# Performance work log

Hardware: AMD Instinct MI355X
Metric: run time of the kernel (lower is better)

Reference implementation:

```python
import jax, jax.numpy as jnp
import numpy as np

BANDWIDTH = 0.1
NUM_ITERS = 5


def setup_inputs() -> dict:
    key = jax.random.key(0)
    # image batch in [0,1], BCHW
    x = jax.random.uniform(key, (2, 3, 96, 96), dtype=jnp.float32)
    return {"x": x}


def reference(x):
    # Mean-shift filtering: each pixel feature y is iteratively moved to the
    # Gaussian-kernel weighted mean of ALL original pixel features:
    #   y_{t+1} = sum_j exp(-||y_t - x_j||^2 / (2 bw^2)) x_j / sum_j exp(...)
    B, C, H, W = x.shape
    N = H * W
    pts = x.reshape(B, C, N).transpose(0, 2, 1)  # [B, N, C] original points
    inv2bw2 = jnp.float32(1.0 / (2.0 * BANDWIDTH * BANDWIDTH))
    x_sq = jnp.sum(pts * pts, axis=-1)  # [B, N]

    def step(y, _):
        # squared pairwise distances via ||y||^2 + ||x||^2 - 2 y.x  -> [B, N, N]
        y_sq = jnp.sum(y * y, axis=-1)  # [B, N]
        d2 = y_sq[:, :, None] + x_sq[:, None, :] - 2.0 * jnp.einsum(
            'bnc,bmc->bnm', y, pts)
        w = jnp.exp(-jnp.maximum(d2, 0.0) * inv2bw2)  # Gaussian kernel weights
        num = jnp.einsum('bnm,bmc->bnc', w, pts)  # weighted sum of points
        den = jnp.sum(w, axis=-1, keepdims=True)  # normalizer (>= 1, self-weight)
        return num / den, None

    y, _ = jax.lax.scan(step, pts, None, length=NUM_ITERS)
    return y.transpose(0, 2, 1).reshape(B, C, H, W)
```

## Files before the change

kernel.cpp:

```cpp
#include <hip/hip_runtime.h>
#include <math.h>


typedef float v2f __attribute__((ext_vector_type(2)));

#define NPTS   9216
#define NB     2
#define TOT    (NB * NPTS)
#define MSPLIT 24
#define SLICE  (NPTS / MSPLIT)
#define WSLICE (SLICE / 4)
#define NPB    256
#define NTILES (NPTS / NPB)
#define LOG2E  1.44269504088896340736f
#define BIASF  217.0f
#define T23F   8388608.0f
#define A2F    -2574068.3f
#define B2F    -666404.1f

__device__ __forceinline__ v2f splat2(float v) { return (v2f){v, v}; }


__global__ __launch_bounds__(256, 4) void ms_iter(const float* __restrict__ x,
                                                  const float4* __restrict__ accIn,
                                                  float4* __restrict__ accOut,
                                                  float s, int first) {
    __shared__ float4 smem[1024];
    float* const xs = (float*)smem;
    float* const ys = xs + SLICE;
    float* const zs = ys + SLICE;
    float* const ws = zs + SLICE;
    float4* const ypar = smem + SLICE;
    float4* const red  = smem;

    const int tid  = threadIdx.x;
    const int lane = tid & 63;
    const int wv   = tid >> 6;
    const int k    = blockIdx.x % MSPLIT;
    const int tile = blockIdx.x / MSPLIT;
    const int b    = tile / NTILES;
    const int nt   = tile - b * NTILES;
    const int nbase = nt * NPB;
    const float* xb = x + b * 3 * NPTS;
    const int mbeg = k * SLICE;

    for (int i = tid; i < SLICE; i += 256) {
        int g = mbeg + i;
        float px = xb[g] * s;
        float py = xb[NPTS + g] * s;
        float pz = xb[2 * NPTS + g] * s;
        xs[i] = 2.f * px;
        ys[i] = 2.f * py;
        zs[i] = 2.f * pz;
        ws[i] = -fmaf(px, px, fmaf(py, py, pz * pz));
    }
    {
        float y0, y1, y2;
        if (first) {
            int n = nbase + tid;
            y0 = xb[n] * s; y1 = xb[NPTS + n] * s; y2 = xb[2 * NPTS + n] * s;
        } else {
            float4 a = accIn[b * NPTS + nbase + tid];
            float inv = 1.0f / a.w;
            y0 = a.x * inv; y1 = a.y * inv; y2 = a.z * inv;
        }
        ypar[tid] = make_float4(y0, y1, y2,
                                BIASF - fmaf(y0, y0, fmaf(y1, y1, y2 * y2)));
    }
    __syncthreads();

    v2f Yx[4], Yy[4], Yz[4], Yw[4], Ax[4], Ay[4], Az[4], Aw[4];
#pragma unroll
    for (int j = 0; j < 4; ++j) {
        float4 yp = ypar[lane + 64 * j];
        Yx[j] = splat2(yp.x); Yy[j] = splat2(yp.y);
        Yz[j] = splat2(yp.z); Yw[j] = splat2(yp.w);
        Ax[j] = splat2(0.f); Ay[j] = splat2(0.f);
        Az[j] = splat2(0.f); Aw[j] = splat2(0.f);
    }

    const float* xsw = xs + wv * WSLICE;
    const float* ysw = ys + wv * WSLICE;
    const float* zsw = zs + wv * WSLICE;
    const float* wsw = ws + wv * WSLICE;

    const v2f T23 = splat2(T23F);
    const v2f A2  = splat2(A2F);
    const v2f B2  = splat2(B2F);

    for (int i = 0; i < WSLICE; i += 4) {
        float4 PX = *(const float4*)(xsw + i);
        float4 PY = *(const float4*)(ysw + i);
        float4 PZ = *(const float4*)(zsw + i);
        float4 PW = *(const float4*)(wsw + i);
        v2f px0 = (v2f){PX.x, PX.y}, px1 = (v2f){PX.z, PX.w};
        v2f py0 = (v2f){PY.x, PY.y}, py1 = (v2f){PY.z, PY.w};
        v2f pz0 = (v2f){PZ.x, PZ.y}, pz1 = (v2f){PZ.z, PZ.w};
        v2f pw0 = (v2f){PW.x, PW.y}, pw1 = (v2f){PW.z, PW.w};
#pragma unroll
        for (int j = 0; j < 4; ++j) {
            v2f t0 = pw0 + Yw[j];
            t0 = __builtin_elementwise_fma(pz0, Yz[j], t0);
            t0 = __builtin_elementwise_fma(py0, Yy[j], t0);
            t0 = __builtin_elementwise_fma(px0, Yx[j], t0);
            v2f t1 = pw1 + Yw[j];
            t1 = __builtin_elementwise_fma(pz1, Yz[j], t1);
            t1 = __builtin_elementwise_fma(py1, Yy[j], t1);
            t1 = __builtin_elementwise_fma(px1, Yx[j], t1);
            v2f f0, f1;
            f0.x = __builtin_amdgcn_fractf(t0.x);
            f0.y = __builtin_amdgcn_fractf(t0.y);
            f1.x = __builtin_amdgcn_fractf(t1.x);
            f1.y = __builtin_amdgcn_fractf(t1.y);
            v2f h0 = __builtin_elementwise_fma(-f0, f0, f0);
            v2f h1 = __builtin_elementwise_fma(-f1, f1, f1);
            v2f c0 = __builtin_elementwise_fma(f0, B2, A2);
            v2f c1 = __builtin_elementwise_fma(f1, B2, A2);
            v2f g0 = h0 * c0;
            v2f g1 = h1 * c1;
            v2f V0 = __builtin_elementwise_fma(t0, T23, g0);
            v2f V1 = __builtin_elementwise_fma(t1, T23, g1);
            v2f w0, w1;
            w0.x = __int_as_float((int)V0.x);
            w0.y = __int_as_float((int)V0.y);
            w1.x = __int_as_float((int)V1.x);
            w1.y = __int_as_float((int)V1.y);
            Ax[j] = __builtin_elementwise_fma(w0, px0, Ax[j]);
            Ay[j] = __builtin_elementwise_fma(w0, py0, Ay[j]);
            Az[j] = __builtin_elementwise_fma(w0, pz0, Az[j]);
            Aw[j] += w0;
            Ax[j] = __builtin_elementwise_fma(w1, px1, Ax[j]);
            Ay[j] = __builtin_elementwise_fma(w1, py1, Ay[j]);
            Az[j] = __builtin_elementwise_fma(w1, pz1, Az[j]);
            Aw[j] += w1;
        }
    }

    __syncthreads();
#pragma unroll
    for (int j = 0; j < 4; ++j) {
        red[wv * NPB + lane + 64 * j] =
            make_float4(Ax[j].x + Ax[j].y, Ay[j].x + Ay[j].y,
                        Az[j].x + Az[j].y, Aw[j].x + Aw[j].y);
    }
    __syncthreads();
    {
        float4 r0 = red[tid];
        float4 r1 = red[NPB + tid];
        float4 r2 = red[2 * NPB + tid];
        float4 r3 = red[3 * NPB + tid];
        float ox = 0.5f * ((r0.x + r1.x) + (r2.x + r3.x));
        float oy = 0.5f * ((r0.y + r1.y) + (r2.y + r3.y));
        float oz = 0.5f * ((r0.z + r1.z) + (r2.z + r3.z));
        float od = (r0.w + r1.w) + (r2.w + r3.w);
        float* dst = (float*)&accOut[b * NPTS + nbase + tid];
        atomicAdd(dst + 0, ox);
        atomicAdd(dst + 1, oy);
        atomicAdd(dst + 2, oz);
        atomicAdd(dst + 3, od);
    }
}

__global__ __launch_bounds__(256) void ms_pack(const float4* __restrict__ acc4,
                                               float* __restrict__ out,
                                               float invs) {
    int gid = blockIdx.x * 256 + threadIdx.x;
    int b = gid / NPTS;
    int n = gid - b * NPTS;
    float4 a = acc4[gid];
    float f = invs / a.w;
    float* ob = out + b * 3 * NPTS;
    ob[n]            = a.x * f;
    ob[NPTS + n]     = a.y * f;
    ob[2 * NPTS + n] = a.z * f;
}

extern "C" void kernel_launch(void* const* d_in, const int* in_sizes, int n_in,
                              void* d_out, int out_size, void* d_ws, size_t ws_size,
                              hipStream_t stream) {
    const float* x = (const float*)d_in[0];
    float* out = (float*)d_out;
    float s = sqrtf(50.0f * LOG2E);

    float4* acc = (float4*)d_ws;

    hipMemsetAsync(acc, 0, (size_t)5 * TOT * sizeof(float4), stream);

    for (int it = 0; it < 5; ++it) {
        const float4* accIn = (it == 0) ? nullptr : acc + (size_t)(it - 1) * TOT;
        ms_iter<<<NB * NTILES * MSPLIT, 256, 0, stream>>>(
            x, accIn, acc + (size_t)it * TOT, s, it == 0 ? 1 : 0);
    }
    ms_pack<<<TOT / 256, 256, 0, stream>>>(acc + (size_t)4 * TOT, out, 1.0f / s);
}
```

Measured before the change: 288.8 us.

## Use hardware exp2 instead of bit-trick exp, prefetch LDS operands, raise M split

Replaces the software exp approximation (fract, polynomial correction, float-to-int bit reinterpretation) with the hardware v_exp_f32 transcendental and drops the bias constant that approximation needed. Adds a software prefetch of the next group of LDS point values, and raises the M-split factor from 24 to 32, giving more, smaller blocks. The transcendental unit has lower throughput than full-rate FMA, so this trades ALU instruction count for transcendental pressure. The prefetch reads 4 floats past the end of each wave's slice on the last iteration, which stays inside the shared buffer but is wasted work.

Result: faster. 236.3 us (-18.2%).

```diff
diff --git a/kernel.cpp b/kernel.cpp
--- a/kernel.cpp
+++ b/kernel.cpp
@@ -7,16 +7,12 @@
 #define NPTS   9216
 #define NB     2
 #define TOT    (NB * NPTS)
-#define MSPLIT 24
+#define MSPLIT 32
 #define SLICE  (NPTS / MSPLIT)
 #define WSLICE (SLICE / 4)
 #define NPB    256
 #define NTILES (NPTS / NPB)
 #define LOG2E  1.44269504088896340736f
-#define BIASF  217.0f
-#define T23F   8388608.0f
-#define A2F    -2574068.3f
-#define B2F    -666404.1f
 
 __device__ __forceinline__ v2f splat2(float v) { return (v2f){v, v}; }
 
@@ -65,7 +61,7 @@
             y0 = a.x * inv; y1 = a.y * inv; y2 = a.z * inv;
         }
         ypar[tid] = make_float4(y0, y1, y2,
-                                BIASF - fmaf(y0, y0, fmaf(y1, y1, y2 * y2)));
+                                -fmaf(y0, y0, fmaf(y1, y1, y2 * y2)));
     }
     __syncthreads();
 
@@ -84,15 +80,15 @@
     const float* zsw = zs + wv * WSLICE;
     const float* wsw = ws + wv * WSLICE;
 
-    const v2f T23 = splat2(T23F);
-    const v2f A2  = splat2(A2F);
-    const v2f B2  = splat2(B2F);
-
+    float4 PX = *(const float4*)(xsw);
+    float4 PY = *(const float4*)(ysw);
+    float4 PZ = *(const float4*)(zsw);
+    float4 PW = *(const float4*)(wsw);
     for (int i = 0; i < WSLICE; i += 4) {
-        float4 PX = *(const float4*)(xsw + i);
-        float4 PY = *(const float4*)(ysw + i);
-        float4 PZ = *(const float4*)(zsw + i);
-        float4 PW = *(const float4*)(wsw + i);
+        float4 NX = *(const float4*)(xsw + i + 4);
+        float4 NY = *(const float4*)(ysw + i + 4);
+        float4 NZ = *(const float4*)(zsw + i + 4);
+        float4 NW = *(const float4*)(wsw + i + 4);
         v2f px0 = (v2f){PX.x, PX.y}, px1 = (v2f){PX.z, PX.w};
         v2f py0 = (v2f){PY.x, PY.y}, py1 = (v2f){PY.z, PY.w};
         v2f pz0 = (v2f){PZ.x, PZ.y}, pz1 = (v2f){PZ.z, PZ.w};
@@ -107,24 +103,11 @@
             t1 = __builtin_elementwise_fma(pz1, Yz[j], t1);
             t1 = __builtin_elementwise_fma(py1, Yy[j], t1);
             t1 = __builtin_elementwise_fma(px1, Yx[j], t1);
-            v2f f0, f1;
-            f0.x = __builtin_amdgcn_fractf(t0.x);
-            f0.y = __builtin_amdgcn_fractf(t0.y);
-            f1.x = __builtin_amdgcn_fractf(t1.x);
-            f1.y = __builtin_amdgcn_fractf(t1.y);
-            v2f h0 = __builtin_elementwise_fma(-f0, f0, f0);
-            v2f h1 = __builtin_elementwise_fma(-f1, f1, f1);
-            v2f c0 = __builtin_elementwise_fma(f0, B2, A2);
-            v2f c1 = __builtin_elementwise_fma(f1, B2, A2);
-            v2f g0 = h0 * c0;
-            v2f g1 = h1 * c1;
-            v2f V0 = __builtin_elementwise_fma(t0, T23, g0);
-            v2f V1 = __builtin_elementwise_fma(t1, T23, g1);
             v2f w0, w1;
-            w0.x = __int_as_float((int)V0.x);
-            w0.y = __int_as_float((int)V0.y);
-            w1.x = __int_as_float((int)V1.x);
-            w1.y = __int_as_float((int)V1.y);
+            w0.x = __builtin_amdgcn_exp2f(t0.x);
+            w0.y = __builtin_amdgcn_exp2f(t0.y);
+            w1.x = __builtin_amdgcn_exp2f(t1.x);
+            w1.y = __builtin_amdgcn_exp2f(t1.y);
             Ax[j] = __builtin_elementwise_fma(w0, px0, Ax[j]);
             Ay[j] = __builtin_elementwise_fma(w0, py0, Ay[j]);
             Az[j] = __builtin_elementwise_fma(w0, pz0, Az[j]);
@@ -134,6 +117,7 @@
             Az[j] = __builtin_elementwise_fma(w1, pz1, Az[j]);
             Aw[j] += w1;
         }
+        PX = NX; PY = NY; PZ = NZ; PW = NW;
     }
 
     __syncthreads();
```
